# Kernel tuning notes

Measured on AMD Instinct MI355X. Metric: run time of the kernel, lower is better.

The kernel has to match this reference:

```python
import jax, jax.numpy as jnp
import numpy as np

N_NODES = 100000
N_EDGES = 1600000
F_IN = 128
UNITS = 128
BN_EPS = 1e-3  # keras BatchNormalization default epsilon


def setup_inputs() -> dict:
    key = jax.random.key(0)
    ks = jax.random.split(key, 9)
    x = jax.random.normal(ks[0], (N_NODES, F_IN), dtype=jnp.float32)
    edge_index = jax.random.randint(ks[1], (2, N_EDGES), 0, N_NODES, dtype=jnp.int32)
    edge_weight = jax.random.uniform(ks[2], (N_EDGES,), dtype=jnp.float32)
    W = jax.random.normal(ks[3], (F_IN, UNITS), dtype=jnp.float32) * (1.0 / np.sqrt(F_IN))
    bias = jax.random.normal(ks[4], (UNITS,), dtype=jnp.float32) * 0.01
    bn_gamma = jax.random.uniform(ks[5], (UNITS,), dtype=jnp.float32)
    bn_beta = jax.random.normal(ks[6], (UNITS,), dtype=jnp.float32) * 0.1
    bn_mean = jax.random.normal(ks[7], (UNITS,), dtype=jnp.float32) * 0.1
    bn_var = jax.random.uniform(ks[8], (UNITS,), dtype=jnp.float32)
    return {"x": x, "edge_index": edge_index, "edge_weight": edge_weight,
            "W": W, "bias": bias, "bn_gamma": bn_gamma, "bn_beta": bn_beta,
            "bn_mean": bn_mean, "bn_var": bn_var}


def reference(x, edge_index, edge_weight, W, bias, bn_gamma, bn_beta, bn_mean, bn_var):
    num_nodes = x.shape[0]
    # Dense feature transform (no bias)
    h = x @ W  # [N, U]
    # Add self-loops with weight 1
    loop = jnp.arange(num_nodes, dtype=edge_index.dtype)
    row = jnp.concatenate([edge_index[0], loop])  # [E+N]
    col = jnp.concatenate([edge_index[1], loop])  # [E+N]
    w = jnp.concatenate([edge_weight, jnp.ones((num_nodes,), edge_weight.dtype)])
    # Symmetric (improved) normalization: D^{-1/2} A D^{-1/2}
    deg = jax.ops.segment_sum(w, row, num_segments=num_nodes)  # [N]
    deg_safe = jnp.where(deg == 0, 1.0, deg)
    dinv = jnp.where(deg == 0, 0.0, jax.lax.rsqrt(deg_safe))
    norm = dinv[row] * w * dinv[col]  # [E+N]
    # Gather -> scale -> scatter-sum
    messages = h[col] * norm[:, None]  # [E+N, U]
    out = jax.ops.segment_sum(messages, row, num_segments=num_nodes)  # [N, U]
    out = out + bias
    # BatchNorm in inference mode (training=None)
    out = bn_gamma * (out - bn_mean) * jax.lax.rsqrt(bn_var + BN_EPS) + bn_beta
    return jax.nn.relu(out)
```

## Files before the change

### kernel.cpp

```cpp
#include <hip/hip_runtime.h>
#include <math.h>

#define N_NODES 100000
#define N_EDGES 1600000
#define F 128
#define BN_EPS 1e-3f
#define NXCD 8
#define N_BINS (N_NODES * NXCD)
#define NS1B ((N_BINS + 1023) / 1024)
#define XCC_ID_GETREG_IMM 63508

__global__ void init_kernel(int* __restrict__ rowcnt,
                            const float* __restrict__ bias,
                            const float* __restrict__ gamma,
                            const float* __restrict__ beta,
                            const float* __restrict__ mean,
                            const float* __restrict__ var,
                            float* __restrict__ scale,
                            float* __restrict__ shift) {
    int i = blockIdx.x * blockDim.x + threadIdx.x;
    if (i < N_BINS) rowcnt[i] = 0;
    if (blockIdx.x == 0 && threadIdx.x < F) {
        int j = threadIdx.x;
        float s = gamma[j] / sqrtf(var[j] + BN_EPS);
        scale[j] = s;
        shift[j] = (bias[j] - mean[j]) * s + beta[j];
    }
}

__global__ void hist_kernel(const int* __restrict__ ei,
                            int* __restrict__ rowcnt,
                            unsigned short* __restrict__ epos) {
    unsigned int xcd = __builtin_amdgcn_s_getreg(XCC_ID_GETREG_IMM) & (NXCD - 1);
    int e = blockIdx.x * blockDim.x + threadIdx.x;
    if (e < N_EDGES) {
        int r = ei[e];
        unsigned int p = __hip_atomic_fetch_add(
            (unsigned int*)&rowcnt[r * NXCD + xcd], 1u,
            __ATOMIC_RELAXED, __HIP_MEMORY_SCOPE_WORKGROUP);
        epos[e] = (unsigned short)((xcd << 13) | (p & 0x1FFFu));
    }
}

__launch_bounds__(256)
__global__ void scan1_kernel(const int* __restrict__ cnt,
                             int* __restrict__ excl,
                             int* __restrict__ bsum) {
    __shared__ int s[256];
    int t = threadIdx.x;
    int base = blockIdx.x * 1024 + t * 4;
    int v0 = (base + 0 < N_BINS) ? cnt[base + 0] : 0;
    int v1 = (base + 1 < N_BINS) ? cnt[base + 1] : 0;
    int v2 = (base + 2 < N_BINS) ? cnt[base + 2] : 0;
    int v3 = (base + 3 < N_BINS) ? cnt[base + 3] : 0;
    int tsum = v0 + v1 + v2 + v3;
    s[t] = tsum;
    __syncthreads();
    #pragma unroll
    for (int off = 1; off < 256; off <<= 1) {
        int x = s[t];
        if (t >= off) x += s[t - off];
        __syncthreads();
        s[t] = x;
        __syncthreads();
    }
    if (t == 255) bsum[blockIdx.x] = s[255];
    int run = s[t] - tsum;
    if (base + 0 < N_BINS) excl[base + 0] = run;
    run += v0;
    if (base + 1 < N_BINS) excl[base + 1] = run;
    run += v1;
    if (base + 2 < N_BINS) excl[base + 2] = run;
    run += v2;
    if (base + 3 < N_BINS) excl[base + 3] = run;
}

__launch_bounds__(256)
__global__ void scan2_kernel(const int* __restrict__ bsum,
                             int* __restrict__ bexcl) {
    __shared__ int s[256];
    int t = threadIdx.x;
    int base = t * 4;
    int v0 = (base + 0 < NS1B) ? bsum[base + 0] : 0;
    int v1 = (base + 1 < NS1B) ? bsum[base + 1] : 0;
    int v2 = (base + 2 < NS1B) ? bsum[base + 2] : 0;
    int v3 = (base + 3 < NS1B) ? bsum[base + 3] : 0;
    int tsum = v0 + v1 + v2 + v3;
    s[t] = tsum;
    __syncthreads();
    #pragma unroll
    for (int off = 1; off < 256; off <<= 1) {
        int x = s[t];
        if (t >= off) x += s[t - off];
        __syncthreads();
        s[t] = x;
        __syncthreads();
    }
    int run = s[t] - tsum;
    if (base + 0 < NS1B) bexcl[base + 0] = run;
    run += v0;
    if (base + 1 < NS1B) bexcl[base + 1] = run;
    run += v1;
    if (base + 2 < NS1B) bexcl[base + 2] = run;
    run += v2;
    if (base + 3 < NS1B) bexcl[base + 3] = run;
}

__global__ void scan3_kernel(int* __restrict__ basep,
                             const int* __restrict__ bexcl) {
    int i = blockIdx.x * blockDim.x + threadIdx.x;
    if (i < N_BINS) basep[i] += bexcl[i >> 10];
    if (i == 0) basep[N_BINS] = N_EDGES;
}

__global__ void scatter_kernel(const int* __restrict__ ei,
                               const unsigned short* __restrict__ epos,
                               const int* __restrict__ basep,
                               int* __restrict__ eid) {
    int e = blockIdx.x * blockDim.x + threadIdx.x;
    if (e < N_EDGES) {
        int r = ei[e];
        unsigned int t = epos[e];
        unsigned int x = t >> 13;
        unsigned int p = t & 0x1FFFu;
        eid[basep[r * NXCD + x] + p] = e;
    }
}

__launch_bounds__(256)
__global__ void degdinv_kernel(const int* __restrict__ basep,
                               const int* __restrict__ eid,
                               const float* __restrict__ ew,
                               float* __restrict__ dinv) {
    int gtid = blockIdx.x * blockDim.x + threadIdx.x;
    int row = gtid >> 6;
    int lane = gtid & 63;
    if (row >= N_NODES) return;
    int beg = basep[row * NXCD];
    int end = basep[row * NXCD + NXCD];
    float s = 0.0f;
    for (int e = beg + lane; e < end; e += 64)
        s += ew[eid[e]];
    #pragma unroll
    for (int off = 32; off > 0; off >>= 1)
        s += __shfl_xor(s, off);
    if (lane == 0)
        dinv[row] = 1.0f / sqrtf(1.0f + s);
}

__launch_bounds__(256)
__global__ void gemm_kernel(const float* __restrict__ x,
                            const float* __restrict__ W,
                            float* __restrict__ h) {
    __shared__ float Wl[F * F];
    int tid = threadIdx.x;
    int r0 = blockIdx.x * 32;

    const float4* W4 = (const float4*)W;
    float4* Wl4 = (float4*)Wl;
    #pragma unroll
    for (int i = 0; i < 16; ++i)
        Wl4[tid + i * 256] = W4[tid + i * 256];
    __syncthreads();

    int wave = tid >> 6;
    int lane = tid & 63;
    int rbase = r0 + wave * 8;

    float2 acc[8];
    #pragma unroll
    for (int r = 0; r < 8; ++r) acc[r] = make_float2(0.0f, 0.0f);

    const float2* Wl2 = (const float2*)Wl;
    const float4* xg = (const float4*)x;

    #pragma unroll 2
    for (int k4 = 0; k4 < 32; ++k4) {
        float4 xv[8];
        #pragma unroll
        for (int r = 0; r < 8; ++r)
            xv[r] = xg[(long)(rbase + r) * 32 + k4];

#define GSTEP(KK, COMP)                                        \
        {                                                      \
            float2 wv = Wl2[(k4 * 4 + KK) * 64 + lane];        \
            _Pragma("unroll")                                  \
            for (int r = 0; r < 8; ++r) {                      \
                acc[r].x += xv[r].COMP * wv.x;                 \
                acc[r].y += xv[r].COMP * wv.y;                 \
            }                                                  \
        }
        GSTEP(0, x) GSTEP(1, y) GSTEP(2, z) GSTEP(3, w)
#undef GSTEP
    }

    #pragma unroll
    for (int r = 0; r < 8; ++r)
        ((float2*)(h + (long)(rbase + r) * F))[lane] = acc[r];
}

__launch_bounds__(256)
__global__ void gather_kernel(const int* __restrict__ basep,
                              const int* __restrict__ eid,
                              const int* __restrict__ ei,
                              const float* __restrict__ ew,
                              const float* __restrict__ dinv,
                              const float* __restrict__ h,
                              const float* __restrict__ scale,
                              const float* __restrict__ shift,
                              float* __restrict__ out) {
    int gtid = blockIdx.x * blockDim.x + threadIdx.x;
    int row = gtid >> 6;
    int lane = gtid & 63;
    if (row >= N_NODES) return;

    int j0 = lane * 2;
    float sc0 = scale[j0], sc1 = scale[j0 + 1];
    float sh0 = shift[j0], sh1 = shift[j0 + 1];

    const float2* h2 = (const float2*)h;
    const int* ei_col = ei + N_EDGES;
    float di = dinv[row];

    float2 hv = h2[(long)row * 64 + lane];
    float2 acc = make_float2(hv.x * di, hv.y * di);

    int beg = basep[row * NXCD];
    int end = basep[row * NXCD + NXCD];
    int cnt = end - beg;

    for (int chunk = 0; chunk < cnt; chunk += 64) {
        int e = chunk + lane;
        int c = 0;
        float nw = 0.0f;
        if (e < cnt) {
            int eidv = eid[beg + e];
            c = ei_col[eidv];
            nw = ew[eidv] * dinv[c];
        }
        int mcnt = min(cnt - chunk, 64);
        for (int j = 0; j < mcnt; ++j) {
            int cj = __builtin_amdgcn_readlane(c, j);
            float nwj = __int_as_float(
                __builtin_amdgcn_readlane(__float_as_int(nw), j));
            float2 cv = h2[(long)cj * 64 + lane];
            acc.x += cv.x * nwj;
            acc.y += cv.y * nwj;
        }
    }
    acc.x *= di;
    acc.y *= di;

    float2 r;
    r.x = fmaxf(acc.x * sc0 + sh0, 0.0f);
    r.y = fmaxf(acc.y * sc1 + sh1, 0.0f);
    ((float2*)out)[(long)row * 64 + lane] = r;
}

extern "C" void kernel_launch(void* const* d_in, const int* in_sizes, int n_in,
                              void* d_out, int out_size, void* d_ws, size_t ws_size,
                              hipStream_t stream) {
    const float* x     = (const float*)d_in[0];
    const int*   ei    = (const int*)d_in[1];
    const float* ew    = (const float*)d_in[2];
    const float* W     = (const float*)d_in[3];
    const float* bias  = (const float*)d_in[4];
    const float* gamma = (const float*)d_in[5];
    const float* beta  = (const float*)d_in[6];
    const float* mean  = (const float*)d_in[7];
    const float* var   = (const float*)d_in[8];
    float* out = (float*)d_out;

    char* ws = (char*)d_ws;
    float*          h      = (float*)(ws);
    int*            basep  = (int*)  (ws + 51200000);
    int*            eid    = (int*)  (ws + 54400016);
    int*            rowcnt = (int*)  (ws + 54400016);
    unsigned short* epos   = (unsigned short*)(ws + 60800016);
    float*          dinv   = (float*)(ws + 64000016);
    int*            bsum   = (int*)  (ws + 64400016);
    int*            bexcl  = (int*)  (ws + 64404112);
    float*          scale  = (float*)(ws + 64408208);
    float*          shift  = (float*)(ws + 64408720);

    int nb_bins  = (N_BINS + 255) / 256;
    int nb_edges = (N_EDGES + 255) / 256;
    int nb_waves = (N_NODES * 64 + 255) / 256;

    init_kernel<<<nb_bins, 256, 0, stream>>>(rowcnt, bias, gamma, beta,
                                             mean, var, scale, shift);
    hist_kernel<<<nb_edges, 256, 0, stream>>>(ei, rowcnt, epos);

    scan1_kernel<<<NS1B, 256, 0, stream>>>(rowcnt, basep, bsum);
    scan2_kernel<<<1, 256, 0, stream>>>(bsum, bexcl);
    scan3_kernel<<<nb_bins, 256, 0, stream>>>(basep, bexcl);

    scatter_kernel<<<nb_edges, 256, 0, stream>>>(ei, epos, basep, eid);

    degdinv_kernel<<<nb_waves, 256, 0, stream>>>(basep, eid, ew, dinv);

    gemm_kernel<<<N_NODES / 32, 256, 0, stream>>>(x, W, h);

    gather_kernel<<<nb_waves, 256, 0, stream>>>(basep, eid, ei, ew, dinv, h,
                                                scale, shift, out);
}
```

Measured before the change: 535.2 us.

## Store h in fp16 and pack sorted (col, weight) pairs in CSR

The GEMM output h is now written as half2, which halves the bytes moved by the random-access neighbour gather. The scatter step now writes (col, weight) pairs into the CSR order directly, instead of edge ids. This removes the double indirection through eid to ei and ew in both the degree pass and the gather. The fp16 storage of h adds rounding error against the fp32 reference, and the workspace layout is reshuffled, with epos aliasing hh.

```diff
diff --git a/kernel.cpp b/kernel.cpp
--- a/kernel.cpp
+++ b/kernel.cpp
@@ -1,4 +1,5 @@
 #include <hip/hip_runtime.h>
+#include <hip/hip_fp16.h>
 #include <math.h>
 
 #define N_NODES 100000
@@ -114,23 +115,25 @@
 }
 
 __global__ void scatter_kernel(const int* __restrict__ ei,
+                               const float* __restrict__ ew,
                                const unsigned short* __restrict__ epos,
                                const int* __restrict__ basep,
-                               int* __restrict__ eid) {
+                               int2* __restrict__ ecw) {
     int e = blockIdx.x * blockDim.x + threadIdx.x;
     if (e < N_EDGES) {
         int r = ei[e];
+        int c = ei[N_EDGES + e];
+        float w = ew[e];
         unsigned int t = epos[e];
         unsigned int x = t >> 13;
         unsigned int p = t & 0x1FFFu;
-        eid[basep[r * NXCD + x] + p] = e;
+        ecw[basep[r * NXCD + x] + p] = make_int2(c, __float_as_int(w));
     }
 }
 
 __launch_bounds__(256)
 __global__ void degdinv_kernel(const int* __restrict__ basep,
-                               const int* __restrict__ eid,
-                               const float* __restrict__ ew,
+                               const int2* __restrict__ ecw,
                                float* __restrict__ dinv) {
     int gtid = blockIdx.x * blockDim.x + threadIdx.x;
     int row = gtid >> 6;
@@ -140,7 +143,7 @@
     int end = basep[row * NXCD + NXCD];
     float s = 0.0f;
     for (int e = beg + lane; e < end; e += 64)
-        s += ew[eid[e]];
+        s += __int_as_float(ecw[e].y);
     #pragma unroll
     for (int off = 32; off > 0; off >>= 1)
         s += __shfl_xor(s, off);
@@ -151,7 +154,7 @@
 __launch_bounds__(256)
 __global__ void gemm_kernel(const float* __restrict__ x,
                             const float* __restrict__ W,
-                            float* __restrict__ h) {
+                            __half2* __restrict__ hh) {
     __shared__ float Wl[F * F];
     int tid = threadIdx.x;
     int r0 = blockIdx.x * 32;
@@ -196,16 +199,14 @@
 
     #pragma unroll
     for (int r = 0; r < 8; ++r)
-        ((float2*)(h + (long)(rbase + r) * F))[lane] = acc[r];
+        hh[(long)(rbase + r) * 64 + lane] = __floats2half2_rn(acc[r].x, acc[r].y);
 }
 
 __launch_bounds__(256)
 __global__ void gather_kernel(const int* __restrict__ basep,
-                              const int* __restrict__ eid,
-                              const int* __restrict__ ei,
-                              const float* __restrict__ ew,
+                              const int2* __restrict__ ecw,
                               const float* __restrict__ dinv,
-                              const float* __restrict__ h,
+                              const __half2* __restrict__ hh,
                               const float* __restrict__ scale,
                               const float* __restrict__ shift,
                               float* __restrict__ out) {
@@ -218,11 +219,9 @@
     float sc0 = scale[j0], sc1 = scale[j0 + 1];
     float sh0 = shift[j0], sh1 = shift[j0 + 1];
 
-    const float2* h2 = (const float2*)h;
-    const int* ei_col = ei + N_EDGES;
     float di = dinv[row];
 
-    float2 hv = h2[(long)row * 64 + lane];
+    float2 hv = __half22float2(hh[(long)row * 64 + lane]);
     float2 acc = make_float2(hv.x * di, hv.y * di);
 
     int beg = basep[row * NXCD];
@@ -234,16 +233,16 @@
         int c = 0;
         float nw = 0.0f;
         if (e < cnt) {
-            int eidv = eid[beg + e];
-            c = ei_col[eidv];
-            nw = ew[eidv] * dinv[c];
+            int2 m = ecw[beg + e];
+            c = m.x;
+            nw = __int_as_float(m.y) * dinv[c];
         }
         int mcnt = min(cnt - chunk, 64);
         for (int j = 0; j < mcnt; ++j) {
             int cj = __builtin_amdgcn_readlane(c, j);
             float nwj = __int_as_float(
                 __builtin_amdgcn_readlane(__float_as_int(nw), j));
-            float2 cv = h2[(long)cj * 64 + lane];
+            float2 cv = __half22float2(hh[(long)cj * 64 + lane]);
             acc.x += cv.x * nwj;
             acc.y += cv.y * nwj;
         }
@@ -272,16 +271,16 @@
     float* out = (float*)d_out;
 
     char* ws = (char*)d_ws;
-    float*          h      = (float*)(ws);
-    int*            basep  = (int*)  (ws + 51200000);
-    int*            eid    = (int*)  (ws + 54400016);
-    int*            rowcnt = (int*)  (ws + 54400016);
-    unsigned short* epos   = (unsigned short*)(ws + 60800016);
-    float*          dinv   = (float*)(ws + 64000016);
-    int*            bsum   = (int*)  (ws + 64400016);
-    int*            bexcl  = (int*)  (ws + 64404112);
-    float*          scale  = (float*)(ws + 64408208);
-    float*          shift  = (float*)(ws + 64408720);
+    __half2*        hh     = (__half2*)(ws);
+    unsigned short* epos   = (unsigned short*)(ws);
+    int*            basep  = (int*)  (ws + 25600000);
+    int2*           ecw    = (int2*) (ws + 28800016);
+    int*            rowcnt = (int*)  (ws + 28800016);
+    float*          dinv   = (float*)(ws + 41600016);
+    int*            bsum   = (int*)  (ws + 42000016);
+    int*            bexcl  = (int*)  (ws + 42004112);
+    float*          scale  = (float*)(ws + 42008208);
+    float*          shift  = (float*)(ws + 42008720);
 
     int nb_bins  = (N_BINS + 255) / 256;
     int nb_edges = (N_EDGES + 255) / 256;
@@ -295,12 +294,12 @@
     scan2_kernel<<<1, 256, 0, stream>>>(bsum, bexcl);
     scan3_kernel<<<nb_bins, 256, 0, stream>>>(basep, bexcl);
 
-    scatter_kernel<<<nb_edges, 256, 0, stream>>>(ei, epos, basep, eid);
-
-    degdinv_kernel<<<nb_waves, 256, 0, stream>>>(basep, eid, ew, dinv);
-
-    gemm_kernel<<<N_NODES / 32, 256, 0, stream>>>(x, W, h);
-
-    gather_kernel<<<nb_waves, 256, 0, stream>>>(basep, eid, ei, ew, dinv, h,
+    scatter_kernel<<<nb_edges, 256, 0, stream>>>(ei, ew, epos, basep, ecw);
+
+    degdinv_kernel<<<nb_waves, 256, 0, stream>>>(basep, ecw, dinv);
+
+    gemm_kernel<<<N_NODES / 32, 256, 0, stream>>>(x, W, hh);
+
+    gather_kernel<<<nb_waves, 256, 0, stream>>>(basep, ecw, dinv, hh,
                                                 scale, shift, out);
 }
```

Result: faster. 456.7 us (-14.7%).
